# Kernel optimization log

Hardware: AMD Instinct MI355X
Metric: run time of the kernel (lower is better)

The kernel has to match this reference:

```python
import jax, jax.numpy as jnp
import numpy as np

B, Himg, Wimg, C = 4, 32, 32, 512
NUM_HEADS = 8
HEAD_DIM = C // NUM_HEADS          # 64
S_PATCH, L_PATCH = 4, 32           # key/value patch, query patch (l_patch == H so q has 1 patch)
SCALE = HEAD_DIM ** -0.5           # original code's self.scale is unset (bug); standard intent


def patchify(a, H, W, p):
    # a: [B, nh, N, hd] with N == H*W  ->  [B, nh, (H//p)*(W//p), p*p, hd]
    b, nh, n, hd = a.shape
    a = a.reshape(b, nh, H // p, p, W // p, p, hd)
    a = a.transpose(0, 1, 2, 4, 3, 5, 6)
    return a.reshape(b, nh, (H // p) * (W // p), p * p, hd)


def setup_inputs() -> dict:
    key = jax.random.key(0)
    ks = jax.random.split(key, 8)
    w_std = C ** -0.5  # keep qk logits O(1) so softmax is non-degenerate
    return {
        "x_s": jax.random.normal(ks[0], (B, Himg * Wimg, C), jnp.float32),
        "x_l": jax.random.normal(ks[1], (B, Himg * Wimg, C), jnp.float32),
        "Wq": jax.random.normal(ks[2], (C, C), jnp.float32) * w_std,
        "bq": jax.random.normal(ks[3], (C,), jnp.float32) * 0.01,
        "Wk": jax.random.normal(ks[4], (C, C), jnp.float32) * w_std,
        "bk": jax.random.normal(ks[5], (C,), jnp.float32) * 0.01,
        "Wv": jax.random.normal(ks[6], (C, C), jnp.float32) * w_std,
        "bv": jax.random.normal(ks[7], (C,), jnp.float32) * 0.01,
        "H": Himg,
        "W": Wimg,
    }


def reference(x_s, x_l, Wq, bq, Wk, bk, Wv, bv, H, W):
    b, n, c = x_s.shape
    # projections + split heads: [B, nh, N, hd]
    q = (x_l @ Wq + bq).reshape(b, n, NUM_HEADS, HEAD_DIM).transpose(0, 2, 1, 3)
    k = (x_s @ Wk + bk).reshape(b, n, NUM_HEADS, HEAD_DIM).transpose(0, 2, 1, 3)
    v = (x_s @ Wv + bv).reshape(b, n, NUM_HEADS, HEAD_DIM).transpose(0, 2, 1, 3)
    q_p = patchify(q, H, W, L_PATCH)   # [B, nh, 1,  L^2, hd]
    k_p = patchify(k, H, W, S_PATCH)   # [B, nh, Ps, s^2, hd]
    v_p = patchify(v, H, W, S_PATCH)   # [B, nh, Ps, s^2, hd]
    # broadcasted windowed cross-attention: [B, nh, Ps, L^2, s^2]
    attn = jnp.matmul(q_p, k_p.swapaxes(-2, -1)) * SCALE
    attn = jax.nn.softmax(attn, axis=-1)
    # dropout p=0.0 -> identity
    return jnp.matmul(attn, v_p)       # [B, nh, Ps, L^2, hd]
```

## Files before the change

kernel.cpp:

```cpp
#include <hip/hip_runtime.h>
#include <hip/hip_bf16.h>

#define NB 4
#define NH 8
#define NPX 1024
#define HD 64
#define CDIM 512
#define M_ROWS 4096
#define PS 64
#define S2 16

typedef __attribute__((ext_vector_type(8))) short bf16x8;
typedef __attribute__((ext_vector_type(4))) short bf16x4;
typedef __attribute__((ext_vector_type(4))) float f32x4;

typedef const __attribute__((address_space(1))) unsigned int* gptr_t;
typedef __attribute__((address_space(3))) unsigned int* lptr_t;

static __device__ __forceinline__ short f2bf(float f) {
    __hip_bfloat16 h = __float2bfloat16(f);
    return *reinterpret_cast<short*>(&h);
}

__global__ void convert_k(const float* __restrict__ xs, const float* __restrict__ xl,
                          const float* __restrict__ Wq, const float* __restrict__ Wk,
                          const float* __restrict__ Wv,
                          short* __restrict__ xl_bf, short* __restrict__ xs_bf,
                          short* __restrict__ WT ) {
    int i = blockIdx.x * blockDim.x + threadIdx.x;
    if (i < 524288) {
        float4 a = ((const float4*)xl)[i];
        float4 b = ((const float4*)xs)[i];
        short4 oa = make_short4(f2bf(a.x), f2bf(a.y), f2bf(a.z), f2bf(a.w));
        short4 ob = make_short4(f2bf(b.x), f2bf(b.y), f2bf(b.z), f2bf(b.w));
        ((short4*)xl_bf)[i] = oa;
        ((short4*)xs_bf)[i] = ob;
    }
    if (i < 786432) {
        int which = i >> 18;
        int j = i & 262143;
        int n = j >> 9, k = j & 511;
        const float* W = which == 0 ? Wq : (which == 1 ? Wk : Wv);
        WT[i] = f2bf(W[k * 512 + n]);
    }
}

__global__ __launch_bounds__(256, 3) void proj_gemm(
    const short* __restrict__ xl_bf, const short* __restrict__ xs_bf,
    const short* __restrict__ WT, const float* __restrict__ bq,
    const float* __restrict__ bk, const float* __restrict__ bv,
    short* __restrict__ qkv) {
    __shared__ __attribute__((aligned(16))) short A_lds[128 * 64];
    __shared__ __attribute__((aligned(16))) short B_lds[64 * 64];
    const int z = blockIdx.z;
    const int m0 = blockIdx.x * 128;
    const int n0 = blockIdx.y * 64;
    const short* A = (z == 0) ? xl_bf : xs_bf;
    const short* WTz = WT + z * 262144;
    const float* bias = (z == 0) ? bq : ((z == 1) ? bk : bv);
    short* out = qkv + (size_t)z * M_ROWS * CDIM;
    const int t = threadIdx.x, w = t >> 6, lane = t & 63;
    const int lr = lane & 15, g = lane >> 4;

    f32x4 acc[2][4] = {};
    for (int kt = 0; kt < 8; ++kt) {
        const int k0 = kt * 64;
#pragma unroll
        for (int r = 0; r < 4; ++r) {
            int c = r * 256 + t;
            int row = c >> 3, sub = c & 7;
            const short* src = A + (size_t)(m0 + row) * CDIM + k0 + ((sub ^ (row & 7)) * 8);
            __builtin_amdgcn_global_load_lds((gptr_t)src,
                (lptr_t)(A_lds + (r * 256 + w * 64) * 8), 16, 0, 0);
        }
#pragma unroll
        for (int r = 0; r < 2; ++r) {
            int c = r * 256 + t;
            int row = c >> 3, sub = c & 7;
            const short* src = WTz + (size_t)(n0 + row) * CDIM + k0 + ((sub ^ (row & 7)) * 8);
            __builtin_amdgcn_global_load_lds((gptr_t)src,
                (lptr_t)(B_lds + (r * 256 + w * 64) * 8), 16, 0, 0);
        }
        __syncthreads();
        bf16x8 afr[2][2], bfr[4][2];
#pragma unroll
        for (int mt = 0; mt < 2; ++mt)
#pragma unroll
            for (int kk = 0; kk < 2; ++kk) {
                int row = w * 32 + mt * 16 + lr;
                int slot = (kk * 4 + g) ^ (row & 7);
                afr[mt][kk] = *(const bf16x8*)(A_lds + row * 64 + slot * 8);
            }
#pragma unroll
        for (int nt = 0; nt < 4; ++nt)
#pragma unroll
            for (int kk = 0; kk < 2; ++kk) {
                int row = nt * 16 + lr;
                int slot = (kk * 4 + g) ^ (row & 7);
                bfr[nt][kk] = *(const bf16x8*)(B_lds + row * 64 + slot * 8);
            }
#pragma unroll
        for (int kk = 0; kk < 2; ++kk)
#pragma unroll
            for (int mt = 0; mt < 2; ++mt)
#pragma unroll
                for (int nt = 0; nt < 4; ++nt)
                    acc[mt][nt] = __builtin_amdgcn_mfma_f32_16x16x32_bf16(
                        afr[mt][kk], bfr[nt][kk], acc[mt][nt], 0, 0, 0);
        __syncthreads();
    }
#pragma unroll
    for (int mt = 0; mt < 2; ++mt) {
#pragma unroll
        for (int nt = 0; nt < 4; ++nt) {
            int col = n0 + nt * 16 + lr;
            float bv_ = bias[col];
            int row0 = m0 + w * 32 + mt * 16 + g * 4;
#pragma unroll
            for (int r = 0; r < 4; ++r)
                out[(size_t)(row0 + r) * CDIM + col] = f2bf(acc[mt][nt][r] + bv_);
        }
    }
}

__global__ void v_trans(const short* __restrict__ v_bf, short* __restrict__ vTp) {
    __shared__ __attribute__((aligned(16))) short lds[16 * 512];
    const int blk = blockIdx.x;
    const int b = blk >> 6, p = blk & 63;
    const int py = p >> 3, px = p & 7;
    const int t = threadIdx.x;
#pragma unroll
    for (int r = 0; r < 4; ++r) {
        int ci = r * 256 + t;
        int s = ci >> 6, c8 = (ci & 63) * 8;
        int n = py * 128 + (s >> 2) * 32 + px * 4 + (s & 3);
        *(bf16x8*)(lds + s * 512 + c8) =
            *(const bf16x8*)(v_bf + (size_t)(b * NPX + n) * CDIM + c8);
    }
    __syncthreads();
    const int h = t >> 5, d0 = (t & 31) * 2;
#pragma unroll
    for (int dd = 0; dd < 2; ++dd) {
        int d = d0 + dd;
        short tmp[16];
#pragma unroll
        for (int s = 0; s < 16; ++s) tmp[s] = lds[s * 512 + h * 64 + d];
        short* dst = vTp + ((size_t)((b * 8 + h) * PS + p) * HD + d) * S2;
        *(bf16x8*)(dst) = *(const bf16x8*)(tmp);
        *(bf16x8*)(dst + 8) = *(const bf16x8*)(tmp + 8);
    }
}

__global__ __launch_bounds__(256, 4) void attn_k(
    const short* __restrict__ q_bf, const short* __restrict__ k_bf,
    const short* __restrict__ vTp, float* __restrict__ out) {
    __shared__ __attribute__((aligned(16))) short k_lds[2][2][S2 * 64];
    __shared__ __attribute__((aligned(16))) short v_lds[2][2][HD * S2];
    __shared__ __attribute__((aligned(16))) float st_lds[4 * 16 * 68];
    const int bid = blockIdx.x;
    const int wid = ((bid & 7) << 7) | (bid >> 3);
    const int bh = wid >> 5;
    const int b = bh >> 3, h = bh & 7;
    const int rem = wid & 31;
    const int qtile = rem >> 1, pg = rem & 1;
    const int t = threadIdx.x, w = t >> 6, lane = t & 63;
    const int lr = lane & 15, g = lane >> 4;
    const int l_loc = qtile * 64 + w * 16 + lr;

    bf16x8 qfr[2];
    {
        const short* qrow = q_bf + (size_t)(b * NPX + l_loc) * CDIM + h * HD;
        qfr[0] = *(const bf16x8*)(qrow + g * 8);
        qfr[1] = *(const bf16x8*)(qrow + 32 + g * 8);
    }
    float* outbh = out + (size_t)bh * PS * NPX * HD;
    const int p0 = pg * 32;
    float* stw = st_lds + w * 1088;
    const int srow = lane >> 4, schunk = lane & 15;

    const int spp = w >> 1;
    const int cid = ((w & 1) << 6) | lane;
    const int ks = cid >> 3, kc = cid & 7;
    const size_t kbase = (size_t)(b * NPX) * CDIM + h * HD;
    const short* vppbase = vTp + (size_t)(bh * PS) * HD * S2;
    short* kdst = &k_lds[0][spp][(w & 1) * 512];
    short* vdst = &v_lds[0][spp][(w & 1) * 512];
    const int kcol = (kc ^ (ks & 7)) * 8;

    auto stage = [&](int gi, int buf) {
        int p = p0 + gi * 2 + spp;
        int py = p >> 3, px = p & 7;
        int n = py * 128 + (ks >> 2) * 32 + px * 4 + (ks & 3);
        const short* ksrc = k_bf + kbase + (size_t)n * CDIM + kcol;
        __builtin_amdgcn_global_load_lds((gptr_t)ksrc,
            (lptr_t)(kdst + buf * 2048), 16, 0, 0);
        const short* vsrc = vppbase + (size_t)p * (HD * S2) + cid * 8;
        __builtin_amdgcn_global_load_lds((gptr_t)vsrc,
            (lptr_t)(vdst + buf * 2048), 16, 0, 0);
    };
    stage(0, 0);
    asm volatile("s_waitcnt vmcnt(0)" ::: "memory");
    __syncthreads();

    for (int si = 0; si < 16; ++si) {
        const int buf = si & 1;
        if (si < 15) stage(si + 1, buf ^ 1);
#pragma unroll
        for (int pp = 0; pp < 2; ++pp) {
            const int p = p0 + si * 2 + pp;
            const short* kb = k_lds[buf][pp];
            bf16x8 kfr0 = *(const bf16x8*)(kb + ((lr * 64 + g * 8) ^ ((lr & 7) << 3)));
            bf16x8 kfr1 = *(const bf16x8*)(kb + ((lr * 64 + 32 + g * 8) ^ ((lr & 7) << 3)));
            const short* vb = v_lds[buf][pp];
            bf16x4 vfr4[4];
#pragma unroll
            for (int dt = 0; dt < 4; ++dt)
                vfr4[dt] = *(const bf16x4*)(vb + (dt * 16 + lr) * S2 + g * 4);

            f32x4 s_acc = {};
            s_acc = __builtin_amdgcn_mfma_f32_16x16x32_bf16(kfr0, qfr[0], s_acc, 0, 0, 0);
            s_acc = __builtin_amdgcn_mfma_f32_16x16x32_bf16(kfr1, qfr[1], s_acc, 0, 0, 0);
            float sv[4];
            float m = -1e30f;
#pragma unroll
            for (int r = 0; r < 4; ++r) { sv[r] = s_acc[r] * 0.125f; m = fmaxf(m, sv[r]); }
            m = fmaxf(m, __shfl_xor(m, 16));
            m = fmaxf(m, __shfl_xor(m, 32));
            float pv[4]; float sum = 0.f;
#pragma unroll
            for (int r = 0; r < 4; ++r) { pv[r] = __expf(sv[r] - m); sum += pv[r]; }
            sum += __shfl_xor(sum, 16);
            sum += __shfl_xor(sum, 32);
            float rs = 1.f / sum;
            bf16x8 pfr = { f2bf(pv[0] * rs), f2bf(pv[1] * rs), f2bf(pv[2] * rs), f2bf(pv[3] * rs),
                           0, 0, 0, 0 };
            f32x4 oacc[4];
#pragma unroll
            for (int dt = 0; dt < 4; ++dt) {
                bf16x8 vfr = { vfr4[dt][0], vfr4[dt][1], vfr4[dt][2], vfr4[dt][3], 0, 0, 0, 0 };
                f32x4 zero = {};
                oacc[dt] = __builtin_amdgcn_mfma_f32_16x16x32_bf16(vfr, pfr, zero, 0, 0, 0);
            }
#pragma unroll
            for (int dt = 0; dt < 4; ++dt)
                *(f32x4*)(stw + lr * 68 + dt * 16 + g * 4) = oacc[dt];
            float* opbase = outbh + ((size_t)p * NPX + qtile * 64 + w * 16) * HD;
#pragma unroll
            for (int u = 0; u < 4; ++u) {
                f32x4 vout = *(const f32x4*)(stw + (u * 4 + srow) * 68 + schunk * 4);
                *(f32x4*)(opbase + (size_t)(u * 4 + srow) * HD + schunk * 4) = vout;
            }
        }
        if (si < 15) {
            asm volatile("s_waitcnt vmcnt(8) lgkmcnt(0)" ::: "memory");
            __builtin_amdgcn_s_barrier();
            __builtin_amdgcn_sched_barrier(0);
        }
    }
}

extern "C" void kernel_launch(void* const* d_in, const int* in_sizes, int n_in,
                              void* d_out, int out_size, void* d_ws, size_t ws_size,
                              hipStream_t stream) {
    const float* x_s = (const float*)d_in[0];
    const float* x_l = (const float*)d_in[1];
    const float* Wq  = (const float*)d_in[2];
    const float* bq  = (const float*)d_in[3];
    const float* Wk  = (const float*)d_in[4];
    const float* bk  = (const float*)d_in[5];
    const float* Wv  = (const float*)d_in[6];
    const float* bv  = (const float*)d_in[7];
    float* out = (float*)d_out;
    char* ws = (char*)d_ws;

    short* xl_bf = (short*)(ws);
    short* xs_bf = (short*)(ws + 4194304);
    short* WT    = (short*)(ws + 8388608);
    short* qkv   = (short*)(ws + 9961472);
    short* q_bf = qkv;
    short* k_bf = qkv + 2097152;
    short* v_bf = qkv + 4194304;
    short* vTp  = (short*)(ws + 22544384);

    convert_k<<<3072, 256, 0, stream>>>(x_s, x_l, Wq, Wk, Wv, xl_bf, xs_bf, WT);
    proj_gemm<<<dim3(32, 8, 3), 256, 0, stream>>>(xl_bf, xs_bf, WT, bq, bk, bv, qkv);
    v_trans<<<256, 256, 0, stream>>>(v_bf, vTp);
    attn_k<<<1024, 256, 0, stream>>>(q_bf, k_bf, vTp, out);
}
```

Baseline: 138.6 us.

## Shrink attention LDS footprint and double grid to raise occupancy

The attention kernel now processes 16 key patches per block instead of 32 and stages one patch per iteration, with waves 0-1 loading K and waves 2-3 loading V. The output staging buffer is cut to an 8-row tile written in two halves. Launch bounds move to 8 blocks per CU and the grid doubles to 2048 blocks. Together this reduces LDS per block so more blocks fit per CU, which is meant to hide memory latency on the output-store-bound loop. The cost is more barriers per patch and smaller, more frequent load batches.

```diff
diff --git a/kernel.cpp b/kernel.cpp
--- a/kernel.cpp
+++ b/kernel.cpp
@@ -151,18 +151,18 @@
     }
 }
 
-__global__ __launch_bounds__(256, 4) void attn_k(
+__global__ __launch_bounds__(256, 8) void attn_k(
     const short* __restrict__ q_bf, const short* __restrict__ k_bf,
     const short* __restrict__ vTp, float* __restrict__ out) {
-    __shared__ __attribute__((aligned(16))) short k_lds[2][2][S2 * 64];
-    __shared__ __attribute__((aligned(16))) short v_lds[2][2][HD * S2];
-    __shared__ __attribute__((aligned(16))) float st_lds[4 * 16 * 68];
+    __shared__ __attribute__((aligned(16))) short k_lds[2][S2 * 64];
+    __shared__ __attribute__((aligned(16))) short v_lds[2][HD * S2];
+    __shared__ __attribute__((aligned(16))) float st_lds[4][8 * 65];
     const int bid = blockIdx.x;
-    const int wid = ((bid & 7) << 7) | (bid >> 3);
-    const int bh = wid >> 5;
+    const int wid = ((bid & 7) << 8) | (bid >> 3);
+    const int bh = wid >> 6;
     const int b = bh >> 3, h = bh & 7;
-    const int rem = wid & 31;
-    const int qtile = rem >> 1, pg = rem & 1;
+    const int rem = wid & 63;
+    const int qtile = rem >> 2, pg = rem & 3;
     const int t = threadIdx.x, w = t >> 6, lane = t & 63;
     const int lr = lane & 15, g = lane >> 4;
     const int l_loc = qtile * 64 + w * 16 + lr;
@@ -174,85 +174,92 @@
         qfr[1] = *(const bf16x8*)(qrow + 32 + g * 8);
     }
     float* outbh = out + (size_t)bh * PS * NPX * HD;
-    const int p0 = pg * 32;
-    float* stw = st_lds + w * 1088;
-    const int srow = lane >> 4, schunk = lane & 15;
-
-    const int spp = w >> 1;
-    const int cid = ((w & 1) << 6) | lane;
-    const int ks = cid >> 3, kc = cid & 7;
+    const int p0 = pg * 16;
+    float* stw = st_lds[w];
+
+    const bool isK = w < 2;
+    const int ch = ((w & 1) << 6) | lane;
+    const int ks = ch >> 3, kc = ch & 7;
     const size_t kbase = (size_t)(b * NPX) * CDIM + h * HD;
-    const short* vppbase = vTp + (size_t)(bh * PS) * HD * S2;
-    short* kdst = &k_lds[0][spp][(w & 1) * 512];
-    short* vdst = &v_lds[0][spp][(w & 1) * 512];
+    const short* vpb = vTp + (size_t)(bh * PS) * HD * S2;
+    short* dstbase = isK ? &k_lds[0][(w & 1) * 512] : &v_lds[0][(w & 1) * 512];
     const int kcol = (kc ^ (ks & 7)) * 8;
 
-    auto stage = [&](int gi, int buf) {
-        int p = p0 + gi * 2 + spp;
-        int py = p >> 3, px = p & 7;
-        int n = py * 128 + (ks >> 2) * 32 + px * 4 + (ks & 3);
-        const short* ksrc = k_bf + kbase + (size_t)n * CDIM + kcol;
-        __builtin_amdgcn_global_load_lds((gptr_t)ksrc,
-            (lptr_t)(kdst + buf * 2048), 16, 0, 0);
-        const short* vsrc = vppbase + (size_t)p * (HD * S2) + cid * 8;
-        __builtin_amdgcn_global_load_lds((gptr_t)vsrc,
-            (lptr_t)(vdst + buf * 2048), 16, 0, 0);
+    auto stage = [&](int p, int buf) {
+        const short* src;
+        if (isK) {
+            int py = p >> 3, px = p & 7;
+            int n = py * 128 + (ks >> 2) * 32 + px * 4 + (ks & 3);
+            src = k_bf + kbase + (size_t)n * CDIM + kcol;
+        } else {
+            src = vpb + (size_t)p * (HD * S2) + ch * 8;
+        }
+        __builtin_amdgcn_global_load_lds((gptr_t)src,
+            (lptr_t)(dstbase + buf * 1024), 16, 0, 0);
     };
-    stage(0, 0);
+    stage(p0, 0);
     asm volatile("s_waitcnt vmcnt(0)" ::: "memory");
     __syncthreads();
 
     for (int si = 0; si < 16; ++si) {
         const int buf = si & 1;
-        if (si < 15) stage(si + 1, buf ^ 1);
-#pragma unroll
-        for (int pp = 0; pp < 2; ++pp) {
-            const int p = p0 + si * 2 + pp;
-            const short* kb = k_lds[buf][pp];
-            bf16x8 kfr0 = *(const bf16x8*)(kb + ((lr * 64 + g * 8) ^ ((lr & 7) << 3)));
-            bf16x8 kfr1 = *(const bf16x8*)(kb + ((lr * 64 + 32 + g * 8) ^ ((lr & 7) << 3)));
-            const short* vb = v_lds[buf][pp];
-            bf16x4 vfr4[4];
-#pragma unroll
-            for (int dt = 0; dt < 4; ++dt)
-                vfr4[dt] = *(const bf16x4*)(vb + (dt * 16 + lr) * S2 + g * 4);
-
-            f32x4 s_acc = {};
-            s_acc = __builtin_amdgcn_mfma_f32_16x16x32_bf16(kfr0, qfr[0], s_acc, 0, 0, 0);
-            s_acc = __builtin_amdgcn_mfma_f32_16x16x32_bf16(kfr1, qfr[1], s_acc, 0, 0, 0);
-            float sv[4];
-            float m = -1e30f;
-#pragma unroll
-            for (int r = 0; r < 4; ++r) { sv[r] = s_acc[r] * 0.125f; m = fmaxf(m, sv[r]); }
-            m = fmaxf(m, __shfl_xor(m, 16));
-            m = fmaxf(m, __shfl_xor(m, 32));
-            float pv[4]; float sum = 0.f;
-#pragma unroll
-            for (int r = 0; r < 4; ++r) { pv[r] = __expf(sv[r] - m); sum += pv[r]; }
-            sum += __shfl_xor(sum, 16);
-            sum += __shfl_xor(sum, 32);
-            float rs = 1.f / sum;
-            bf16x8 pfr = { f2bf(pv[0] * rs), f2bf(pv[1] * rs), f2bf(pv[2] * rs), f2bf(pv[3] * rs),
-                           0, 0, 0, 0 };
-            f32x4 oacc[4];
-#pragma unroll
-            for (int dt = 0; dt < 4; ++dt) {
-                bf16x8 vfr = { vfr4[dt][0], vfr4[dt][1], vfr4[dt][2], vfr4[dt][3], 0, 0, 0, 0 };
-                f32x4 zero = {};
-                oacc[dt] = __builtin_amdgcn_mfma_f32_16x16x32_bf16(vfr, pfr, zero, 0, 0, 0);
-            }
-#pragma unroll
-            for (int dt = 0; dt < 4; ++dt)
-                *(f32x4*)(stw + lr * 68 + dt * 16 + g * 4) = oacc[dt];
-            float* opbase = outbh + ((size_t)p * NPX + qtile * 64 + w * 16) * HD;
-#pragma unroll
-            for (int u = 0; u < 4; ++u) {
-                f32x4 vout = *(const f32x4*)(stw + (u * 4 + srow) * 68 + schunk * 4);
-                *(f32x4*)(opbase + (size_t)(u * 4 + srow) * HD + schunk * 4) = vout;
+        const int p = p0 + si;
+        if (si < 15) stage(p + 1, buf ^ 1);
+        const short* kb = k_lds[buf];
+        bf16x8 kfr0 = *(const bf16x8*)(kb + ((lr * 64 + g * 8) ^ ((lr & 7) << 3)));
+        bf16x8 kfr1 = *(const bf16x8*)(kb + ((lr * 64 + 32 + g * 8) ^ ((lr & 7) << 3)));
+        const short* vb = v_lds[buf];
+        bf16x4 vfr4[4];
+#pragma unroll
+        for (int dt = 0; dt < 4; ++dt)
+            vfr4[dt] = *(const bf16x4*)(vb + (dt * 16 + lr) * S2 + g * 4);
+
+        f32x4 s_acc = {};
+        s_acc = __builtin_amdgcn_mfma_f32_16x16x32_bf16(kfr0, qfr[0], s_acc, 0, 0, 0);
+        s_acc = __builtin_amdgcn_mfma_f32_16x16x32_bf16(kfr1, qfr[1], s_acc, 0, 0, 0);
+        float sv[4];
+        float m = -1e30f;
+#pragma unroll
+        for (int r = 0; r < 4; ++r) { sv[r] = s_acc[r] * 0.125f; m = fmaxf(m, sv[r]); }
+        m = fmaxf(m, __shfl_xor(m, 16));
+        m = fmaxf(m, __shfl_xor(m, 32));
+        float pv[4]; float sum = 0.f;
+#pragma unroll
+        for (int r = 0; r < 4; ++r) { pv[r] = __expf(sv[r] - m); sum += pv[r]; }
+        sum += __shfl_xor(sum, 16);
+        sum += __shfl_xor(sum, 32);
+        float rs = 1.f / sum;
+        bf16x8 pfr = { f2bf(pv[0] * rs), f2bf(pv[1] * rs), f2bf(pv[2] * rs), f2bf(pv[3] * rs),
+                       0, 0, 0, 0 };
+        f32x4 oacc[4];
+#pragma unroll
+        for (int dt = 0; dt < 4; ++dt) {
+            bf16x8 vfr = { vfr4[dt][0], vfr4[dt][1], vfr4[dt][2], vfr4[dt][3], 0, 0, 0, 0 };
+            f32x4 zero = {};
+            oacc[dt] = __builtin_amdgcn_mfma_f32_16x16x32_bf16(vfr, pfr, zero, 0, 0, 0);
+        }
+        float* opbase = outbh + ((size_t)p * NPX + qtile * 64 + w * 16) * HD;
+#pragma unroll
+        for (int u = 0; u < 2; ++u) {
+            asm volatile("s_waitcnt lgkmcnt(0)" ::: "memory");
+            __builtin_amdgcn_sched_barrier(0);
+            if ((lr >> 3) == u) {
+#pragma unroll
+                for (int dt = 0; dt < 4; ++dt)
+                    *(f32x4*)(stw + (lr & 7) * 65 + dt * 16 + g * 4) = oacc[dt];
+            }
+            asm volatile("s_waitcnt lgkmcnt(0)" ::: "memory");
+            __builtin_amdgcn_sched_barrier(0);
+#pragma unroll
+            for (int j = 0; j < 2; ++j) {
+                int rib = 4 * j + (lane >> 4);
+                f32x4 vout = *(const f32x4*)(stw + rib * 65 + (lane & 15) * 4);
+                int row = u * 8 + rib;
+                *(f32x4*)(opbase + (size_t)row * HD + (lane & 15) * 4) = vout;
             }
         }
         if (si < 15) {
-            asm volatile("s_waitcnt vmcnt(8) lgkmcnt(0)" ::: "memory");
+            asm volatile("s_waitcnt vmcnt(4) lgkmcnt(0)" ::: "memory");
             __builtin_amdgcn_s_barrier();
             __builtin_amdgcn_sched_barrier(0);
         }
@@ -285,5 +292,5 @@
     convert_k<<<3072, 256, 0, stream>>>(x_s, x_l, Wq, Wk, Wv, xl_bf, xs_bf, WT);
     proj_gemm<<<dim3(32, 8, 3), 256, 0, stream>>>(xl_bf, xs_bf, WT, bq, bk, bv, qkv);
     v_trans<<<256, 256, 0, stream>>>(v_bf, vTp);
-    attn_k<<<1024, 256, 0, stream>>>(q_bf, k_bf, vTp, out);
-}
+    attn_k<<<2048, 256, 0, stream>>>(q_bf, k_bf, vTp, out);
+}
```

Measured after the change: 182.7 us. 31.8% more time.
